# Performance work log

Measured on AMD Instinct MI355X. Metric: run time of the kernel, lower is better.

## Reference

```python
import jax, jax.numpy as jnp
import numpy as np

BETA = 0.25  # commitment cost (original code's undefined self.betas)


def setup_inputs() -> dict:
    key = jax.random.key(0)
    k1, k2 = jax.random.split(key)
    B, D, H, W = 32, 256, 32, 32
    K = 1024
    x = jax.random.normal(k1, (B, D, H, W), dtype=jnp.float32)
    # nn.Embedding init: uniform(-1/K, 1/K)
    emb = jax.random.uniform(k2, (K, D), dtype=jnp.float32,
                             minval=-1.0 / K, maxval=1.0 / K)
    return {"x": x, "emb": emb}


def reference(x, emb):
    # x: [B, D, H, W] -> NHWC
    xp = jnp.transpose(x, (0, 2, 3, 1))          # [B, H, W, D]
    D = emb.shape[1]
    z = xp.reshape(-1, D)                        # [N, D]
    # pairwise squared distance: ||z||^2 + ||e||^2 - 2 z e^T
    dist = (jnp.sum(z * z, axis=1, keepdims=True)
            + jnp.sum(emb * emb, axis=1)
            - 2.0 * jnp.einsum('nd,kd->nk', z, emb))  # [N, K]
    idx = jnp.argmin(dist, axis=1)               # [N] int
    z_quant = emb[idx].reshape(xp.shape)         # [B, H, W, D]
    sg = jax.lax.stop_gradient
    loss = (jnp.mean((sg(z_quant) - xp) ** 2)
            + BETA * jnp.mean((z_quant - sg(xp)) ** 2))
    # straight-through estimator
    z_quant = xp + sg(z_quant - xp)
    z_quant = jnp.transpose(z_quant, (0, 3, 1, 2))  # back to NCHW
    return z_quant, idx, loss
```

## Files before the change

kernel.cpp:

```cpp
#include <hip/hip_runtime.h>

typedef _Float16 half8 __attribute__((ext_vector_type(8)));
typedef _Float16 half4v __attribute__((ext_vector_type(4)));
typedef float f32x4 __attribute__((ext_vector_type(4)));

#define ZQ_ELEMS 8388608
#define N_TOK    32768
#define D_DIM    256
#define K_CB     1024

#define FLAG_CAP 8192
#define ESCALE   1024.0f
#define TAU      0.15f

__device__ __align__(16) _Float16 g_eh[K_CB * D_DIM];
__device__ __align__(16) float g_ebT[D_DIM * K_CB];
__device__ float g_ck[K_CB];
__device__ float g_bk[K_CB];
__device__ float g_loss;
__device__ int   g_cnt;
__device__ int   g_flags[FLAG_CAP];
__device__ float g_zst[FLAG_CAP * 256];
__device__ float g_aA[FLAG_CAP];
__device__ unsigned long long g_best[FLAG_CAP];

__device__ __forceinline__ unsigned long long enc_dk(float D, int k) {
  unsigned int b = __float_as_uint(D);
  unsigned int u = (b & 0x80000000u) ? ~b : (b | 0x80000000u);
  return (((unsigned long long)u) << 32) | (unsigned int)k;
}

__global__ __launch_bounds__(256) void vq_prep(const float* __restrict__ emb) {
  const int tid = threadIdx.x;
  const int w   = tid >> 6;
  const int l   = tid & 63;
  const int k   = (blockIdx.x << 2) + w;
  f32x4 v = *(const f32x4*)(emb + (k << 8) + (l << 2));
  double sd = (double)v[0]*v[0] + (double)v[1]*v[1] + (double)v[2]*v[2] + (double)v[3]*v[3];
  #pragma unroll
  for (int m = 1; m < 64; m <<= 1) sd += __shfl_xor(sd, m);
  if (l == 0) { g_bk[k] = (float)sd; g_ck[k] = 512.0f * (float)sd; }
  half4v h;
  h[0] = (_Float16)(v[0] * ESCALE); h[1] = (_Float16)(v[1] * ESCALE);
  h[2] = (_Float16)(v[2] * ESCALE); h[3] = (_Float16)(v[3] * ESCALE);
  *(half4v*)(g_eh + (k << 8) + (l << 2)) = h;
  const int gi = blockIdx.x * 256 + tid;
  if (gi < FLAG_CAP) g_best[gi] = ~0ULL;
  if (blockIdx.x == 0 && tid == 0) { g_loss = 0.0f; g_cnt = 0; }
}

__global__ __launch_bounds__(256) void vq_tr(const float* __restrict__ emb) {
  __shared__ float tl[64][65];
  const int tx = threadIdx.x & 63, ty = threadIdx.x >> 6;
  const int k0 = (blockIdx.x & 15) << 6;
  const int d0 = (blockIdx.x >> 4) << 6;
  #pragma unroll
  for (int j = 0; j < 16; j++) {
    const int kk = (ty << 4) + j;
    tl[kk][tx] = emb[((k0 + kk) << 8) + d0 + tx];
  }
  __syncthreads();
  #pragma unroll
  for (int j = 0; j < 16; j++) {
    const int dd = (ty << 4) + j;
    g_ebT[((d0 + dd) << 10) + k0 + tx] = tl[tx][dd];
  }
}

__global__ __launch_bounds__(256, 2) void vq_main(const float* __restrict__ x,
                                                  const float* __restrict__ emb,
                                                  float* __restrict__ out) {
  __shared__ __align__(16) _Float16 zt[64 * 256];
  __shared__ float ckl[K_CB];
  __shared__ float wv1[4][64], wv2[4][64];
  __shared__ int   wi1[4][64];
  __shared__ int   fidx[64];
  __shared__ float lred[4];

  const int tid = threadIdx.x;
  const int n0  = blockIdx.x * 64;
  const int b   = blockIdx.x >> 4;
  const int hw0 = (blockIdx.x & 15) << 6;

  #pragma unroll
  for (int i = 0; i < 4; i++) ckl[tid + 256 * i] = g_ck[tid + 256 * i];

  {
    const int hw8 = (tid & 7) << 3;
    const int dl  = tid >> 3;
    #pragma unroll
    for (int it = 0; it < 8; it++) {
      const int d = (it << 5) + dl;
      const float* src = x + (((b << 8) + d) << 10) + hw0 + hw8;
      f32x4 a0 = *(const f32x4*)src;
      f32x4 a1 = *(const f32x4*)(src + 4);
      _Float16 cv[8];
      cv[0]=(_Float16)a0[0]; cv[1]=(_Float16)a0[1]; cv[2]=(_Float16)a0[2]; cv[3]=(_Float16)a0[3];
      cv[4]=(_Float16)a1[0]; cv[5]=(_Float16)a1[1]; cv[6]=(_Float16)a1[2]; cv[7]=(_Float16)a1[3];
      const int blkx = d >> 3;
      #pragma unroll
      for (int i = 0; i < 8; i++) {
        const int n   = hw8 + i;
        const int blk = blkx ^ i ^ (tid & 7);
        zt[(n << 8) + (blk << 3) + (d & 7)] = cv[i];
      }
    }
  }
  __syncthreads();

  const int w = tid >> 6;
  const int l = tid & 63;
  const int c = l & 15;
  const int q = l >> 4;

  half8 af[4][8];
  #pragma unroll
  for (int t = 0; t < 4; t++) {
    const int n  = (t << 4) + c;
    const int sw = (n & 7) ^ (n >> 3);
    #pragma unroll
    for (int s = 0; s < 8; s++) {
      const int K = (s << 2) + q;
      af[t][s] = *(const half8*)(zt + (n << 8) + ((K ^ sw) << 3));
    }
  }

  float v1[4][4], v2[4][4]; int i1[4][4];
  #pragma unroll
  for (int t = 0; t < 4; t++)
    #pragma unroll
    for (int r = 0; r < 4; r++) { v1[t][r] = -3e38f; v2[t][r] = -3e38f; i1[t][r] = 0; }

  for (int jj = 0; jj < 16; jj++) {
    const int k0 = (w << 4) + (jj << 6);
    const float ckv = ckl[k0 + c];
    f32x4 acc[4];
    #pragma unroll
    for (int t = 0; t < 4; t++) acc[t] = f32x4{-ckv, -ckv, -ckv, -ckv};
    #pragma unroll
    for (int s = 0; s < 8; s++) {
      const half8 bf = *(const half8*)(g_eh + ((k0 + c) << 8) + (s << 5) + (q << 3));
      #pragma unroll
      for (int t = 0; t < 4; t++)
        acc[t] = __builtin_amdgcn_mfma_f32_16x16x32_f16(af[t][s], bf, acc[t], 0, 0, 0);
    }
    const int kk = k0 + c;
    #pragma unroll
    for (int t = 0; t < 4; t++)
      #pragma unroll
      for (int r = 0; r < 4; r++) {
        const float sv = acc[t][r];
        if (sv > v1[t][r]) { v2[t][r] = v1[t][r]; v1[t][r] = sv; i1[t][r] = kk; }
        else if (sv > v2[t][r]) v2[t][r] = sv;
      }
  }

  #pragma unroll
  for (int t = 0; t < 4; t++)
    #pragma unroll
    for (int r = 0; r < 4; r++) {
      float a1v = v1[t][r], a2v = v2[t][r]; int ai = i1[t][r];
      #pragma unroll
      for (int m = 8; m >= 1; m >>= 1) {
        const float o1 = __shfl_xor(a1v, m);
        const int   oi = __shfl_xor(ai, m);
        const float o2 = __shfl_xor(a2v, m);
        if (o1 > a1v || (o1 == a1v && oi < ai)) { a2v = fmaxf(a1v, o2); a1v = o1; ai = oi; }
        else a2v = fmaxf(a2v, o1);
      }
      if (c == 0) {
        const int nl = (t << 4) + (q << 2) + r;
        wv1[w][nl] = a1v; wv2[w][nl] = a2v; wi1[w][nl] = ai;
      }
    }
  __syncthreads();

  if (tid < 64) {
    float a1v = wv1[0][tid], a2v = wv2[0][tid]; int ai = wi1[0][tid];
    #pragma unroll
    for (int ww = 1; ww < 4; ww++) {
      const float o1 = wv1[ww][tid]; const int oi = wi1[ww][tid]; const float o2 = wv2[ww][tid];
      if (o1 > a1v || (o1 == a1v && oi < ai)) { a2v = fmaxf(a1v, o2); a1v = o1; ai = oi; }
      else a2v = fmaxf(a2v, o1);
    }
    fidx[tid] = ai;
    out[ZQ_ELEMS + n0 + tid] = (float)ai;
    if (a1v - a2v < TAU) {
      int p = atomicAdd(&g_cnt, 1);
      if (p < FLAG_CAP) g_flags[p] = n0 + tid;
    }
  }
  __syncthreads();

  float lacc = 0.0f;
  {
    const int hw = tid & 63;
    const int sw = (hw & 7) ^ (hw >> 3);
    const float* erow = emb + (fidx[hw] << 8);
    #pragma unroll
    for (int it = 0; it < 8; it++) {
      const int dblk = (it << 2) + w;
      half8 zv = *(const half8*)(zt + (hw << 8) + ((dblk ^ sw) << 3));
      f32x4 e0 = *(const f32x4*)(erow + (dblk << 3));
      f32x4 e1 = *(const f32x4*)(erow + (dblk << 3) + 4);
      #pragma unroll
      for (int j = 0; j < 8; j++) {
        const int d = (dblk << 3) + j;
        const float ef = (j < 4) ? e0[j] : e1[j - 4];
        const float df = ef - (float)zv[j];
        lacc += df * df;
        out[(((b << 8) + d) << 10) + hw0 + hw] = ef;
      }
    }
  }
  #pragma unroll
  for (int m = 1; m < 64; m <<= 1) lacc += __shfl_xor(lacc, m);
  if (l == 0) lred[w] = lacc;
  __syncthreads();
  if (tid == 0) atomicAdd(&g_loss, lred[0] + lred[1] + lred[2] + lred[3]);
}

__global__ __launch_bounds__(256) void vq_stage(const float* __restrict__ x) {
  __shared__ float zl[256];
  const int tid = threadIdx.x;
  int cnt = g_cnt; if (cnt > FLAG_CAP) cnt = FLAG_CAP;
  for (int s = blockIdx.x; s < cnt; s += gridDim.x) {
    const int n = g_flags[s], b = n >> 10, hw = n & 1023;
    const float zv = x[(((b << 8) + tid) << 10) + hw];
    g_zst[(s << 8) + tid] = zv;
    zl[tid] = zv;
    __syncthreads();
    if (tid < 32) {
      double sa = 0.0;
      #pragma unroll
      for (int j = 0; j < 8; j++) { const double z = (double)zl[(tid << 3) + j]; sa += z * z; }
      #pragma unroll
      for (int m = 1; m < 32; m <<= 1) sa += __shfl_xor(sa, m);
      if (tid == 0) g_aA[s] = (float)sa;
    }
    __syncthreads();
  }
}

__global__ __launch_bounds__(256) void vq_fix() {
  __shared__ float z0l[256], z1l[256];
  __shared__ float bvv[2][256];
  __shared__ int   bkk[2][256];
  const int tid = threadIdx.x;
  int cnt = g_cnt; if (cnt > FLAG_CAP) cnt = FLAG_CAP;
  const int njob = ((cnt + 1) >> 1) << 2;
  for (int j = blockIdx.x; j < njob; j += gridDim.x) {
    const int pr = j >> 2, r = j & 3;
    const int s0 = pr << 1;
    const int s1 = (s0 + 1 < cnt) ? s0 + 1 : cnt - 1;
    z0l[tid] = g_zst[(s0 << 8) + tid];
    z1l[tid] = g_zst[(s1 << 8) + tid];
    __syncthreads();
    double c0 = 0.0, c1 = 0.0;
    const float* colbase = g_ebT + (r << 8) + tid;
    #pragma unroll 8
    for (int d = 0; d < 256; d++) {
      const double e = (double)colbase[d << 10];
      c0 = fma(e, (double)z0l[d], c0);
      c1 = fma(e, (double)z1l[d], c1);
    }
    const int k = (r << 8) + tid;
    const float bkv = g_bk[k];
    bvv[0][tid] = (g_aA[s0] + bkv) - 2.0f * (float)c0;
    bkk[0][tid] = k;
    bvv[1][tid] = (g_aA[s1] + bkv) - 2.0f * (float)c1;
    bkk[1][tid] = k;
    __syncthreads();
    for (int off = 128; off >= 1; off >>= 1) {
      if (tid < off) {
        #pragma unroll
        for (int g = 0; g < 2; g++) {
          const float v2c = bvv[g][tid + off]; const int k2 = bkk[g][tid + off];
          if (v2c < bvv[g][tid] || (v2c == bvv[g][tid] && k2 < bkk[g][tid])) {
            bvv[g][tid] = v2c; bkk[g][tid] = k2;
          }
        }
      }
      __syncthreads();
    }
    if (tid == 0) {
      atomicMin(&g_best[s0], enc_dk(bvv[0][0], bkk[0][0]));
      atomicMin(&g_best[s1], enc_dk(bvv[1][0], bkk[1][0]));
    }
    __syncthreads();
  }
}

__global__ __launch_bounds__(256) void vq_out(float* __restrict__ out) {
  int cnt = g_cnt; if (cnt > FLAG_CAP) cnt = FLAG_CAP;
  for (int s = blockIdx.x * 256 + threadIdx.x; s < cnt; s += gridDim.x * 256)
    out[ZQ_ELEMS + g_flags[s]] = (float)(unsigned int)(g_best[s] & 0xFFFFFFFFu);
}

__global__ void vq_fin(float* __restrict__ out) {
  out[ZQ_ELEMS + N_TOK] = g_loss * (1.25f / 8388608.0f);
}

extern "C" void kernel_launch(void* const* d_in, const int* in_sizes, int n_in,
                              void* d_out, int out_size, void* d_ws, size_t ws_size,
                              hipStream_t stream) {
  const float* x   = (const float*)d_in[0];
  const float* emb = (const float*)d_in[1];
  float* out = (float*)d_out;
  vq_prep<<<256, 256, 0, stream>>>(emb);
  vq_tr<<<64, 256, 0, stream>>>(emb);
  vq_main<<<512, 256, 0, stream>>>(x, emb, out);
  vq_stage<<<1024, 256, 0, stream>>>(x);
  vq_fix<<<2048, 256, 0, stream>>>();
  vq_out<<<32, 256, 0, stream>>>(out);
  vq_fin<<<1, 1, 0, stream>>>(out);
}
```

Baseline: 198.5 us.

## Fuse VQ kernels, halve main tile to 32 tokens, patch z_q for refined indices

Merges the codebook transpose into the prep kernel and the flagged-token staging into the main kernel. The loss finalisation moves into the output kernel, so seven launches become four. The main kernel now handles 32 tokens per block across 1024 blocks with a higher occupancy hint, which adds parallelism at the cost of less reuse of codebook fragments. The output kernel now rewrites z_q rows for tokens whose refined index changed, which fixes z_q consistency. It also adds serial per-flag staging inside main blocks.

```diff
diff --git a/kernel.cpp b/kernel.cpp
--- a/kernel.cpp
+++ b/kernel.cpp
@@ -31,6 +31,7 @@
 }
 
 __global__ __launch_bounds__(256) void vq_prep(const float* __restrict__ emb) {
+  __shared__ float tl[64][65];
   const int tid = threadIdx.x;
   const int w   = tid >> 6;
   const int l   = tid & 63;
@@ -47,50 +48,52 @@
   const int gi = blockIdx.x * 256 + tid;
   if (gi < FLAG_CAP) g_best[gi] = ~0ULL;
   if (blockIdx.x == 0 && tid == 0) { g_loss = 0.0f; g_cnt = 0; }
-}
-
-__global__ __launch_bounds__(256) void vq_tr(const float* __restrict__ emb) {
-  __shared__ float tl[64][65];
-  const int tx = threadIdx.x & 63, ty = threadIdx.x >> 6;
-  const int k0 = (blockIdx.x & 15) << 6;
-  const int d0 = (blockIdx.x >> 4) << 6;
-  #pragma unroll
-  for (int j = 0; j < 16; j++) {
-    const int kk = (ty << 4) + j;
-    tl[kk][tx] = emb[((k0 + kk) << 8) + d0 + tx];
-  }
-  __syncthreads();
-  #pragma unroll
-  for (int j = 0; j < 16; j++) {
-    const int dd = (ty << 4) + j;
-    g_ebT[((d0 + dd) << 10) + k0 + tx] = tl[tx][dd];
-  }
-}
-
-__global__ __launch_bounds__(256, 2) void vq_main(const float* __restrict__ x,
+  if (blockIdx.x < 64) {
+    const int tx = tid & 63, ty = tid >> 6;
+    const int k0 = (blockIdx.x & 15) << 6;
+    const int d0 = (blockIdx.x >> 4) << 6;
+    #pragma unroll
+    for (int j = 0; j < 16; j++) {
+      const int kk = (ty << 4) + j;
+      tl[kk][tx] = emb[((k0 + kk) << 8) + d0 + tx];
+    }
+    __syncthreads();
+    #pragma unroll
+    for (int j = 0; j < 16; j++) {
+      const int dd = (ty << 4) + j;
+      g_ebT[((d0 + dd) << 10) + k0 + tx] = tl[tx][dd];
+    }
+  }
+}
+
+__global__ __launch_bounds__(256, 4) void vq_main(const float* __restrict__ x,
                                                   const float* __restrict__ emb,
                                                   float* __restrict__ out) {
-  __shared__ __align__(16) _Float16 zt[64 * 256];
+  __shared__ __align__(16) _Float16 zt[32 * 256];
   __shared__ float ckl[K_CB];
-  __shared__ float wv1[4][64], wv2[4][64];
-  __shared__ int   wi1[4][64];
-  __shared__ int   fidx[64];
+  __shared__ float wv1[4][32], wv2[4][32];
+  __shared__ int   wi1[4][32];
+  __shared__ int   fidx[32];
   __shared__ float lred[4];
+  __shared__ int   fcnt;
+  __shared__ int   fslot[32], ftok[32];
 
   const int tid = threadIdx.x;
-  const int n0  = blockIdx.x * 64;
-  const int b   = blockIdx.x >> 4;
-  const int hw0 = (blockIdx.x & 15) << 6;
+  const int n0  = blockIdx.x << 5;
+  const int b   = blockIdx.x >> 5;
+  const int hw0 = (blockIdx.x & 31) << 5;
+
+  if (tid == 0) fcnt = 0;
 
   #pragma unroll
   for (int i = 0; i < 4; i++) ckl[tid + 256 * i] = g_ck[tid + 256 * i];
 
   {
-    const int hw8 = (tid & 7) << 3;
-    const int dl  = tid >> 3;
-    #pragma unroll
-    for (int it = 0; it < 8; it++) {
-      const int d = (it << 5) + dl;
+    const int hw8 = (tid & 3) << 3;
+    const int dl  = tid >> 2;
+    #pragma unroll
+    for (int it = 0; it < 4; it++) {
+      const int d = (it << 6) + dl;
       const float* src = x + (((b << 8) + d) << 10) + hw0 + hw8;
       f32x4 a0 = *(const f32x4*)src;
       f32x4 a1 = *(const f32x4*)(src + 4);
@@ -101,7 +104,7 @@
       #pragma unroll
       for (int i = 0; i < 8; i++) {
         const int n   = hw8 + i;
-        const int blk = blkx ^ i ^ (tid & 7);
+        const int blk = blkx ^ i ^ (tid & 3);
         zt[(n << 8) + (blk << 3) + (d & 7)] = cv[i];
       }
     }
@@ -113,9 +116,9 @@
   const int c = l & 15;
   const int q = l >> 4;
 
-  half8 af[4][8];
-  #pragma unroll
-  for (int t = 0; t < 4; t++) {
+  half8 af[2][8];
+  #pragma unroll
+  for (int t = 0; t < 2; t++) {
     const int n  = (t << 4) + c;
     const int sw = (n & 7) ^ (n >> 3);
     #pragma unroll
@@ -125,28 +128,27 @@
     }
   }
 
-  float v1[4][4], v2[4][4]; int i1[4][4];
-  #pragma unroll
-  for (int t = 0; t < 4; t++)
+  float v1[2][4], v2[2][4]; int i1[2][4];
+  #pragma unroll
+  for (int t = 0; t < 2; t++)
     #pragma unroll
     for (int r = 0; r < 4; r++) { v1[t][r] = -3e38f; v2[t][r] = -3e38f; i1[t][r] = 0; }
 
   for (int jj = 0; jj < 16; jj++) {
     const int k0 = (w << 4) + (jj << 6);
     const float ckv = ckl[k0 + c];
-    f32x4 acc[4];
-    #pragma unroll
-    for (int t = 0; t < 4; t++) acc[t] = f32x4{-ckv, -ckv, -ckv, -ckv};
+    f32x4 acc[2];
+    acc[0] = f32x4{-ckv, -ckv, -ckv, -ckv};
+    acc[1] = f32x4{-ckv, -ckv, -ckv, -ckv};
     #pragma unroll
     for (int s = 0; s < 8; s++) {
       const half8 bf = *(const half8*)(g_eh + ((k0 + c) << 8) + (s << 5) + (q << 3));
-      #pragma unroll
-      for (int t = 0; t < 4; t++)
-        acc[t] = __builtin_amdgcn_mfma_f32_16x16x32_f16(af[t][s], bf, acc[t], 0, 0, 0);
+      acc[0] = __builtin_amdgcn_mfma_f32_16x16x32_f16(af[0][s], bf, acc[0], 0, 0, 0);
+      acc[1] = __builtin_amdgcn_mfma_f32_16x16x32_f16(af[1][s], bf, acc[1], 0, 0, 0);
     }
     const int kk = k0 + c;
     #pragma unroll
-    for (int t = 0; t < 4; t++)
+    for (int t = 0; t < 2; t++)
       #pragma unroll
       for (int r = 0; r < 4; r++) {
         const float sv = acc[t][r];
@@ -156,7 +158,7 @@
   }
 
   #pragma unroll
-  for (int t = 0; t < 4; t++)
+  for (int t = 0; t < 2; t++)
     #pragma unroll
     for (int r = 0; r < 4; r++) {
       float a1v = v1[t][r], a2v = v2[t][r]; int ai = i1[t][r];
@@ -175,7 +177,7 @@
     }
   __syncthreads();
 
-  if (tid < 64) {
+  if (tid < 32) {
     float a1v = wv1[0][tid], a2v = wv2[0][tid]; int ai = wi1[0][tid];
     #pragma unroll
     for (int ww = 1; ww < 4; ww++) {
@@ -187,19 +189,24 @@
     out[ZQ_ELEMS + n0 + tid] = (float)ai;
     if (a1v - a2v < TAU) {
       int p = atomicAdd(&g_cnt, 1);
-      if (p < FLAG_CAP) g_flags[p] = n0 + tid;
+      if (p < FLAG_CAP) {
+        g_flags[p] = n0 + tid;
+        int lp = atomicAdd(&fcnt, 1);
+        fslot[lp] = p; ftok[lp] = n0 + tid;
+      }
     }
   }
   __syncthreads();
 
   float lacc = 0.0f;
   {
-    const int hw = tid & 63;
+    const int hw = tid & 31;
+    const int g  = tid >> 5;
     const int sw = (hw & 7) ^ (hw >> 3);
     const float* erow = emb + (fidx[hw] << 8);
     #pragma unroll
-    for (int it = 0; it < 8; it++) {
-      const int dblk = (it << 2) + w;
+    for (int it = 0; it < 4; it++) {
+      const int dblk = (it << 3) + g;
       half8 zv = *(const half8*)(zt + (hw << 8) + ((dblk ^ sw) << 3));
       f32x4 e0 = *(const f32x4*)(erow + (dblk << 3));
       f32x4 e1 = *(const f32x4*)(erow + (dblk << 3) + 4);
@@ -218,22 +225,20 @@
   if (l == 0) lred[w] = lacc;
   __syncthreads();
   if (tid == 0) atomicAdd(&g_loss, lred[0] + lred[1] + lred[2] + lred[3]);
-}
-
-__global__ __launch_bounds__(256) void vq_stage(const float* __restrict__ x) {
-  __shared__ float zl[256];
-  const int tid = threadIdx.x;
-  int cnt = g_cnt; if (cnt > FLAG_CAP) cnt = FLAG_CAP;
-  for (int s = blockIdx.x; s < cnt; s += gridDim.x) {
-    const int n = g_flags[s], b = n >> 10, hw = n & 1023;
-    const float zv = x[(((b << 8) + tid) << 10) + hw];
+
+  const int nf = fcnt;
+  for (int f = 0; f < nf; f++) {
+    const int s = fslot[f];
+    const int n = ftok[f];
+    const int bb = n >> 10, hw = n & 1023;
+    const float zv = x[(((bb << 8) + tid) << 10) + hw];
     g_zst[(s << 8) + tid] = zv;
-    zl[tid] = zv;
+    ckl[tid] = zv;
     __syncthreads();
     if (tid < 32) {
       double sa = 0.0;
       #pragma unroll
-      for (int j = 0; j < 8; j++) { const double z = (double)zl[(tid << 3) + j]; sa += z * z; }
+      for (int j = 0; j < 8; j++) { const double z = (double)ckl[(tid << 3) + j]; sa += z * z; }
       #pragma unroll
       for (int m = 1; m < 32; m <<= 1) sa += __shfl_xor(sa, m);
       if (tid == 0) g_aA[s] = (float)sa;
@@ -291,14 +296,23 @@
   }
 }
 
-__global__ __launch_bounds__(256) void vq_out(float* __restrict__ out) {
+__global__ __launch_bounds__(256) void vq_out(const float* __restrict__ emb,
+                                              float* __restrict__ out) {
+  const int tid = threadIdx.x;
+  if (blockIdx.x == 0 && tid == 0)
+    out[ZQ_ELEMS + N_TOK] = g_loss * (1.25f / 8388608.0f);
   int cnt = g_cnt; if (cnt > FLAG_CAP) cnt = FLAG_CAP;
-  for (int s = blockIdx.x * 256 + threadIdx.x; s < cnt; s += gridDim.x * 256)
-    out[ZQ_ELEMS + g_flags[s]] = (float)(unsigned int)(g_best[s] & 0xFFFFFFFFu);
-}
-
-__global__ void vq_fin(float* __restrict__ out) {
-  out[ZQ_ELEMS + N_TOK] = g_loss * (1.25f / 8388608.0f);
+  for (int s = blockIdx.x; s < cnt; s += gridDim.x) {
+    const int n = g_flags[s];
+    const int kw = (int)(unsigned int)(g_best[s] & 0xFFFFFFFFu);
+    const int kold = (int)out[ZQ_ELEMS + n];
+    __syncthreads();
+    if (tid == 0) out[ZQ_ELEMS + n] = (float)kw;
+    if (kw != kold) {
+      const int bb = n >> 10, hw = n & 1023;
+      out[(((bb << 8) + tid) << 10) + hw] = emb[(kw << 8) + tid];
+    }
+  }
 }
 
 extern "C" void kernel_launch(void* const* d_in, const int* in_sizes, int n_in,
@@ -308,10 +322,7 @@
   const float* emb = (const float*)d_in[1];
   float* out = (float*)d_out;
   vq_prep<<<256, 256, 0, stream>>>(emb);
-  vq_tr<<<64, 256, 0, stream>>>(emb);
-  vq_main<<<512, 256, 0, stream>>>(x, emb, out);
-  vq_stage<<<1024, 256, 0, stream>>>(x);
-  vq_fix<<<2048, 256, 0, stream>>>();
-  vq_out<<<32, 256, 0, stream>>>(out);
-  vq_fin<<<1, 1, 0, stream>>>(out);
-}
+  vq_main<<<1024, 256, 0, stream>>>(x, emb, out);
+  vq_fix<<<1536, 256, 0, stream>>>();
+  vq_out<<<256, 256, 0, stream>>>(emb, out);
+}
```

New measurement: 225.0 us. +13.3%, slower.

## Fuse VQ pipeline kernels and use wave-shuffle argmin in exact refinement

Applied to the files above, without the earlier changes.

Merges the codebook transpose into the prep kernel and moves staging of flagged tokens into the tail of the main kernel. This cuts the launch count from seven to four. The exact fp64 refinement kernel now uses four independent accumulators per token and a wave shuffle plus cross-wave argmin in place of a shared-memory tree reduction. The output kernel also writes the loss and patches the quantized output rows for tokens whose refined index changed, which the code before did not do. The staging work inside the main kernel runs serially per block and reuses the ckl shared buffer, adding a tail to vq_main.

```diff
diff --git a/kernel.cpp b/kernel.cpp
--- a/kernel.cpp
+++ b/kernel.cpp
@@ -12,6 +12,8 @@
 #define FLAG_CAP 8192
 #define ESCALE   1024.0f
 #define TAU      0.15f
+#define FIX_GRID 2048
+#define OUT_GRID 512
 
 __device__ __align__(16) _Float16 g_eh[K_CB * D_DIM];
 __device__ __align__(16) float g_ebT[D_DIM * K_CB];
@@ -31,6 +33,7 @@
 }
 
 __global__ __launch_bounds__(256) void vq_prep(const float* __restrict__ emb) {
+  __shared__ float tl[64][65];
   const int tid = threadIdx.x;
   const int w   = tid >> 6;
   const int l   = tid & 63;
@@ -47,23 +50,21 @@
   const int gi = blockIdx.x * 256 + tid;
   if (gi < FLAG_CAP) g_best[gi] = ~0ULL;
   if (blockIdx.x == 0 && tid == 0) { g_loss = 0.0f; g_cnt = 0; }
-}
-
-__global__ __launch_bounds__(256) void vq_tr(const float* __restrict__ emb) {
-  __shared__ float tl[64][65];
-  const int tx = threadIdx.x & 63, ty = threadIdx.x >> 6;
-  const int k0 = (blockIdx.x & 15) << 6;
-  const int d0 = (blockIdx.x >> 4) << 6;
-  #pragma unroll
-  for (int j = 0; j < 16; j++) {
-    const int kk = (ty << 4) + j;
-    tl[kk][tx] = emb[((k0 + kk) << 8) + d0 + tx];
-  }
-  __syncthreads();
-  #pragma unroll
-  for (int j = 0; j < 16; j++) {
-    const int dd = (ty << 4) + j;
-    g_ebT[((d0 + dd) << 10) + k0 + tx] = tl[tx][dd];
+  if (blockIdx.x < 64) {
+    const int tx = tid & 63, ty = tid >> 6;
+    const int k0 = (blockIdx.x & 15) << 6;
+    const int d0 = (blockIdx.x >> 4) << 6;
+    #pragma unroll
+    for (int j = 0; j < 16; j++) {
+      const int kk = (ty << 4) + j;
+      tl[kk][tx] = emb[((k0 + kk) << 8) + d0 + tx];
+    }
+    __syncthreads();
+    #pragma unroll
+    for (int j = 0; j < 16; j++) {
+      const int dd = (ty << 4) + j;
+      g_ebT[((d0 + dd) << 10) + k0 + tx] = tl[tx][dd];
+    }
   }
 }
 
@@ -76,11 +77,15 @@
   __shared__ int   wi1[4][64];
   __shared__ int   fidx[64];
   __shared__ float lred[4];
+  __shared__ int   fcnt;
+  __shared__ int   fslot[64], ftok[64];
 
   const int tid = threadIdx.x;
   const int n0  = blockIdx.x * 64;
   const int b   = blockIdx.x >> 4;
   const int hw0 = (blockIdx.x & 15) << 6;
+
+  if (tid == 0) fcnt = 0;
 
   #pragma unroll
   for (int i = 0; i < 4; i++) ckl[tid + 256 * i] = g_ck[tid + 256 * i];
@@ -187,7 +192,11 @@
     out[ZQ_ELEMS + n0 + tid] = (float)ai;
     if (a1v - a2v < TAU) {
       int p = atomicAdd(&g_cnt, 1);
-      if (p < FLAG_CAP) g_flags[p] = n0 + tid;
+      if (p < FLAG_CAP) {
+        g_flags[p] = n0 + tid;
+        int lp = atomicAdd(&fcnt, 1);
+        fslot[lp] = p; ftok[lp] = n0 + tid;
+      }
     }
   }
   __syncthreads();
@@ -218,22 +227,20 @@
   if (l == 0) lred[w] = lacc;
   __syncthreads();
   if (tid == 0) atomicAdd(&g_loss, lred[0] + lred[1] + lred[2] + lred[3]);
-}
-
-__global__ __launch_bounds__(256) void vq_stage(const float* __restrict__ x) {
-  __shared__ float zl[256];
-  const int tid = threadIdx.x;
-  int cnt = g_cnt; if (cnt > FLAG_CAP) cnt = FLAG_CAP;
-  for (int s = blockIdx.x; s < cnt; s += gridDim.x) {
-    const int n = g_flags[s], b = n >> 10, hw = n & 1023;
-    const float zv = x[(((b << 8) + tid) << 10) + hw];
+
+  const int nf = fcnt;
+  for (int f = 0; f < nf; f++) {
+    const int s = fslot[f];
+    const int n = ftok[f];
+    const int bb = n >> 10, hw = n & 1023;
+    const float zv = x[(((bb << 8) + tid) << 10) + hw];
     g_zst[(s << 8) + tid] = zv;
-    zl[tid] = zv;
+    ckl[tid] = zv;
     __syncthreads();
     if (tid < 32) {
       double sa = 0.0;
       #pragma unroll
-      for (int j = 0; j < 8; j++) { const double z = (double)zl[(tid << 3) + j]; sa += z * z; }
+      for (int j = 0; j < 8; j++) { const double z = (double)ckl[(tid << 3) + j]; sa += z * z; }
       #pragma unroll
       for (int m = 1; m < 32; m <<= 1) sa += __shfl_xor(sa, m);
       if (tid == 0) g_aA[s] = (float)sa;
@@ -242,10 +249,10 @@
   }
 }
 
-__global__ __launch_bounds__(256) void vq_fix() {
+__global__ __launch_bounds__(256, 2) void vq_fix() {
   __shared__ float z0l[256], z1l[256];
-  __shared__ float bvv[2][256];
-  __shared__ int   bkk[2][256];
+  __shared__ float rv[2][4];
+  __shared__ int   rk[2][4];
   const int tid = threadIdx.x;
   int cnt = g_cnt; if (cnt > FLAG_CAP) cnt = FLAG_CAP;
   const int njob = ((cnt + 1) >> 1) << 2;
@@ -256,49 +263,74 @@
     z0l[tid] = g_zst[(s0 << 8) + tid];
     z1l[tid] = g_zst[(s1 << 8) + tid];
     __syncthreads();
-    double c0 = 0.0, c1 = 0.0;
+    double a0 = 0.0, a1 = 0.0, a2 = 0.0, a3 = 0.0;
+    double b0 = 0.0, b1 = 0.0, b2 = 0.0, b3 = 0.0;
     const float* colbase = g_ebT + (r << 8) + tid;
     #pragma unroll 8
-    for (int d = 0; d < 256; d++) {
-      const double e = (double)colbase[d << 10];
-      c0 = fma(e, (double)z0l[d], c0);
-      c1 = fma(e, (double)z1l[d], c1);
-    }
+    for (int i = 0; i < 64; i++) {
+      const double e0 = (double)colbase[(i      ) << 10];
+      const double e1 = (double)colbase[(i +  64) << 10];
+      const double e2 = (double)colbase[(i + 128) << 10];
+      const double e3 = (double)colbase[(i + 192) << 10];
+      a0 = fma(e0, (double)z0l[i      ], a0);
+      a1 = fma(e1, (double)z0l[i +  64], a1);
+      a2 = fma(e2, (double)z0l[i + 128], a2);
+      a3 = fma(e3, (double)z0l[i + 192], a3);
+      b0 = fma(e0, (double)z1l[i      ], b0);
+      b1 = fma(e1, (double)z1l[i +  64], b1);
+      b2 = fma(e2, (double)z1l[i + 128], b2);
+      b3 = fma(e3, (double)z1l[i + 192], b3);
+    }
+    const double c0 = (a0 + a1) + (a2 + a3);
+    const double c1 = (b0 + b1) + (b2 + b3);
     const int k = (r << 8) + tid;
     const float bkv = g_bk[k];
-    bvv[0][tid] = (g_aA[s0] + bkv) - 2.0f * (float)c0;
-    bkk[0][tid] = k;
-    bvv[1][tid] = (g_aA[s1] + bkv) - 2.0f * (float)c1;
-    bkk[1][tid] = k;
-    __syncthreads();
-    for (int off = 128; off >= 1; off >>= 1) {
-      if (tid < off) {
-        #pragma unroll
-        for (int g = 0; g < 2; g++) {
-          const float v2c = bvv[g][tid + off]; const int k2 = bkk[g][tid + off];
-          if (v2c < bvv[g][tid] || (v2c == bvv[g][tid] && k2 < bkk[g][tid])) {
-            bvv[g][tid] = v2c; bkk[g][tid] = k2;
-          }
-        }
-      }
-      __syncthreads();
-    }
+    float v0 = (g_aA[s0] + bkv) - 2.0f * (float)c0;
+    float v1 = (g_aA[s1] + bkv) - 2.0f * (float)c1;
+    int k0i = k, k1i = k;
+    #pragma unroll
+    for (int m = 1; m < 64; m <<= 1) {
+      const float o0 = __shfl_xor(v0, m); const int x0 = __shfl_xor(k0i, m);
+      const float o1 = __shfl_xor(v1, m); const int x1 = __shfl_xor(k1i, m);
+      if (o0 < v0 || (o0 == v0 && x0 < k0i)) { v0 = o0; k0i = x0; }
+      if (o1 < v1 || (o1 == v1 && x1 < k1i)) { v1 = o1; k1i = x1; }
+    }
+    const int wv = tid >> 6;
+    if ((tid & 63) == 0) { rv[0][wv] = v0; rk[0][wv] = k0i; rv[1][wv] = v1; rk[1][wv] = k1i; }
+    __syncthreads();
     if (tid == 0) {
-      atomicMin(&g_best[s0], enc_dk(bvv[0][0], bkk[0][0]));
-      atomicMin(&g_best[s1], enc_dk(bvv[1][0], bkk[1][0]));
-    }
-    __syncthreads();
-  }
-}
-
-__global__ __launch_bounds__(256) void vq_out(float* __restrict__ out) {
+      float fb0 = rv[0][0]; int fk0 = rk[0][0];
+      float fb1 = rv[1][0]; int fk1 = rk[1][0];
+      #pragma unroll
+      for (int ww = 1; ww < 4; ww++) {
+        if (rv[0][ww] < fb0 || (rv[0][ww] == fb0 && rk[0][ww] < fk0)) { fb0 = rv[0][ww]; fk0 = rk[0][ww]; }
+        if (rv[1][ww] < fb1 || (rv[1][ww] == fb1 && rk[1][ww] < fk1)) { fb1 = rv[1][ww]; fk1 = rk[1][ww]; }
+      }
+      atomicMin(&g_best[s0], enc_dk(fb0, fk0));
+      atomicMin(&g_best[s1], enc_dk(fb1, fk1));
+    }
+    __syncthreads();
+  }
+}
+
+__global__ __launch_bounds__(256) void vq_out(const float* __restrict__ emb,
+                                              float* __restrict__ out) {
+  const int tid = threadIdx.x;
+  if (blockIdx.x == 0 && tid == 0)
+    out[ZQ_ELEMS + N_TOK] = g_loss * (1.25f / 8388608.0f);
   int cnt = g_cnt; if (cnt > FLAG_CAP) cnt = FLAG_CAP;
-  for (int s = blockIdx.x * 256 + threadIdx.x; s < cnt; s += gridDim.x * 256)
-    out[ZQ_ELEMS + g_flags[s]] = (float)(unsigned int)(g_best[s] & 0xFFFFFFFFu);
-}
-
-__global__ void vq_fin(float* __restrict__ out) {
-  out[ZQ_ELEMS + N_TOK] = g_loss * (1.25f / 8388608.0f);
+  for (int s = blockIdx.x; s < cnt; s += gridDim.x) {
+    const int n = g_flags[s];
+    const int kw = (int)(unsigned int)(g_best[s] & 0xFFFFFFFFu);
+    const int kold = (int)out[ZQ_ELEMS + n];
+    __syncthreads();
+    if (tid == 0) out[ZQ_ELEMS + n] = (float)kw;
+    if (kw != kold) {
+      const int bb = n >> 10, hw = n & 1023;
+      out[(((bb << 8) + tid) << 10) + hw] = emb[(kw << 8) + tid];
+    }
+    __syncthreads();
+  }
 }
 
 extern "C" void kernel_launch(void* const* d_in, const int* in_sizes, int n_in,
@@ -308,10 +340,7 @@
   const float* emb = (const float*)d_in[1];
   float* out = (float*)d_out;
   vq_prep<<<256, 256, 0, stream>>>(emb);
-  vq_tr<<<64, 256, 0, stream>>>(emb);
   vq_main<<<512, 256, 0, stream>>>(x, emb, out);
-  vq_stage<<<1024, 256, 0, stream>>>(x);
-  vq_fix<<<2048, 256, 0, stream>>>();
-  vq_out<<<32, 256, 0, stream>>>(out);
-  vq_fin<<<1, 1, 0, stream>>>(out);
-}
+  vq_fix<<<FIX_GRID, 256, 0, stream>>>();
+  vq_out<<<OUT_GRID, 256, 0, stream>>>(emb, out);
+}
```

After: 204.4 us. 3.0% more time.
